# Optimization experiments

Hardware: AMD Instinct MI355X
Metric: run time of the kernel (lower is better)

The kernel has to match this reference:

```python
import jax, jax.numpy as jnp
import numpy as np

PAD = 0
C_CONST = 0.1712209


def setup_inputs() -> dict:
    key = jax.random.key(0)
    ks = jax.random.split(key, 6)
    tlen, bsz, slen, hsize, vocab = 64, 32, 64, 1024, 32000
    hidden = jax.random.normal(ks[0], (tlen, bsz, hsize), dtype=jnp.float32)
    context = jax.random.normal(ks[1], (slen, bsz, hsize), dtype=jnp.float32)
    src = jax.random.randint(ks[2], (bsz, slen), 0, vocab, dtype=jnp.int64)
    stdv = 1.0 / np.sqrt(hsize)
    W_gen = jax.random.uniform(ks[3], (vocab, hsize), dtype=jnp.float32, minval=-stdv, maxval=stdv)
    b_gen = jnp.zeros((vocab,), dtype=jnp.float32)
    # Xavier-like init for the copy gate
    w_copy = jax.random.normal(ks[4], (hsize,), dtype=jnp.float32) * np.sqrt(2.0 / (hsize + 1))
    b_copy = jnp.zeros((1,), dtype=jnp.float32)
    return {"hidden": hidden, "context": context, "src": src,
            "W_gen": W_gen, "b_gen": b_gen, "w_copy": w_copy, "b_copy": b_copy}


def reference(hidden, context, src, W_gen, b_gen, w_copy, b_copy):
    tlen, bsz, hsize = hidden.shape
    # p(z=1): probability of copying, [tlen, bsz, 1]
    copy_prob = jax.nn.sigmoid(jnp.einsum('tbh,h->tb', hidden, w_copy) + b_copy[0])[..., None]
    # generator distribution over tgt vocab
    logits = jnp.einsum('tbh,vh->tbv', hidden, W_gen) + b_gen
    prob = jax.nn.softmax(logits.astype(jnp.float32), axis=-1)
    p_g = prob * (1.0 - copy_prob)  # [tlen, bsz, vocab]
    # copy attention over source positions: bmm(query[b,t,h], keys[b,s,h]^T)
    attn_score = jnp.einsum('tbh,sbh->bts', hidden, context)  # [bsz, tlen, slen]
    src_mask = (src == PAD)[:, None, :]  # [bsz, 1, slen]
    attn_score = jnp.where(src_mask, -jnp.inf, attn_score.astype(jnp.float32))
    attns = jax.nn.softmax(attn_score, axis=-1)  # [bsz, tlen, slen]
    p_c = jnp.transpose(attns, (1, 0, 2)) * copy_prob  # [tlen, bsz, slen]
    # scatter_add copy probs into vocab distribution along dim 2
    slen = src.shape[1]
    idx_src = jnp.broadcast_to(src[None, :, :], (tlen, bsz, slen))
    t_idx = jnp.arange(tlen)[:, None, None]
    b_idx = jnp.arange(bsz)[None, :, None]
    p_g = p_g.at[t_idx, b_idx, idx_src].add(p_c)
    return jnp.log(p_g) + C_CONST
```

## Files before the change

### kernel.cpp

```cpp
#include <hip/hip_runtime.h>
#include <hip/hip_bf16.h>
#include <stdint.h>

#define TLEN 64
#define BSZ 32
#define SLEN 64
#define HS 1024
#define VOC 32000
#define NROW (TLEN*BSZ)
#define C_CONST_F 0.1712209f

#define BM 256
#define BN 256
#define BKT 32
#define NKT (HS/BKT)
#define SLOT_BYTES 32768
#define B_REGION 16384

typedef __attribute__((ext_vector_type(8))) short short8;
typedef __attribute__((ext_vector_type(4))) float f32x4;

static __device__ __forceinline__ ushort f2bf(float f) {
    uint32_t u = __builtin_bit_cast(uint32_t, f);
    uint32_t r = (u + 0x7fffu + ((u >> 16) & 1u)) >> 16;
    return (ushort)r;
}
static __device__ __forceinline__ float bf2f(ushort u) {
    uint32_t v = ((uint32_t)u) << 16;
    return __builtin_bit_cast(float, v);
}
static __device__ __forceinline__ void async16(const void* g, void* lds) {
    __builtin_amdgcn_global_load_lds(
        (const __attribute__((address_space(1))) void*)g,
        (__attribute__((address_space(3))) void*)lds, 16, 0, 0);
}
static __device__ __forceinline__ int swz12(int e) { return e ^ (((e >> 4) & 15) << 1); }

__global__ __launch_bounds__(256) void gate_kernel(const float* __restrict__ hidden,
                                                   const float* __restrict__ w_copy,
                                                   const float* __restrict__ b_copy,
                                                   float* __restrict__ cp) {
    int wid = threadIdx.x >> 6, lane = threadIdx.x & 63;
    int row = blockIdx.x * 4 + wid;
    const float* h = hidden + (size_t)row * HS;
    float acc = 0.f;
    for (int i = 0; i < 4; ++i) {
        int off = (i * 64 + lane) * 4;
        float4 a = *(const float4*)(h + off);
        float4 w = *(const float4*)(w_copy + off);
        acc += a.x * w.x + a.y * w.y + a.z * w.z + a.w * w.w;
    }
    for (int m = 32; m >= 1; m >>= 1) acc += __shfl_xor(acc, m, 64);
    if (lane == 0) cp[row] = 1.f / (1.f + expf(-(acc + b_copy[0])));
}

__global__ __launch_bounds__(256) void attn_kernel(const float* __restrict__ hidden,
                                                   const float* __restrict__ context,
                                                   const int* __restrict__ src,
                                                   const float* __restrict__ cp,
                                                   float* __restrict__ p_c) {
    int row = blockIdx.x;
    int b = row & (BSZ - 1);
    int tid = threadIdx.x, wid = tid >> 6, lane = tid & 63;
    __shared__ float hrow[HS];
    __shared__ float sc[SLEN];
    *(float4*)(hrow + tid * 4) = *(const float4*)(hidden + (size_t)row * HS + tid * 4);
    __syncthreads();
    for (int j = 0; j < 16; ++j) {
        int s = wid * 16 + j;
        const float* c = context + ((size_t)s * BSZ + b) * HS;
        float acc = 0.f;
        for (int i = 0; i < 4; ++i) {
            int off = (i * 64 + lane) * 4;
            float4 cv = *(const float4*)(c + off);
            float4 hv = *(const float4*)(hrow + off);
            acc += cv.x * hv.x + cv.y * hv.y + cv.z * hv.z + cv.w * hv.w;
        }
        for (int m = 32; m >= 1; m >>= 1) acc += __shfl_xor(acc, m, 64);
        if (lane == 0) sc[s] = acc;
    }
    __syncthreads();
    if (tid < SLEN) {
        float v = sc[tid];
        if (src[b * SLEN + tid] == 0) v = -INFINITY;
        float m = v;
        for (int k = 32; k >= 1; k >>= 1) m = fmaxf(m, __shfl_xor(m, k, 64));
        float e = expf(v - m);
        float ssum = e;
        for (int k = 32; k >= 1; k >>= 1) ssum += __shfl_xor(ssum, k, 64);
        p_c[row * SLEN + tid] = (e / ssum) * cp[row];
    }
}

__global__ __launch_bounds__(256) void cvt_kernel(const float* __restrict__ in,
                                                  ushort* __restrict__ out, int n4) {
    int i = blockIdx.x * blockDim.x + threadIdx.x;
    if (i >= n4) return;
    float4 v = ((const float4*)in)[i];
    ushort4 o;
    o.x = f2bf(v.x); o.y = f2bf(v.y); o.z = f2bf(v.z); o.w = f2bf(v.w);
    ((ushort4*)out)[i] = o;
}

template <bool BF16L>
__global__ __launch_bounds__(512, 2) void gemm_kernel(const ushort* __restrict__ A,
                                                      const ushort* __restrict__ B,
                                                      const float* __restrict__ b_gen,
                                                      void* __restrict__ logits,
                                                      float* __restrict__ partials ) {
    __shared__ ushort sAB[4 * SLOT_BYTES / 2];

    int orig = blockIdx.x;
    int wg = (orig & 7) * 125 + (orig >> 3);
    int mIdx = wg & 7;
    int nIdx = wg >> 3;
    int m0 = mIdx * BM, n0 = nIdx * BN;
    int tid = threadIdx.x, wid = tid >> 6, lane = tid & 63;
    int wm = (wid >> 2) * 128, wn = (wid & 3) * 64;
    int lr = lane & 15, lg = lane >> 4;

    const ushort* gA[2]; const ushort* gB[2];
    uint32_t ldsOffA[2], ldsOffB[2];
    #pragma unroll
    for (int j = 0; j < 2; ++j) {
        int s = j * 512 + tid;
        int row = s >> 2;
        int kc = (s & 3) ^ ((row >> 1) & 3);
        gA[j] = A + (size_t)(m0 + row) * HS + kc * 8;
        gB[j] = B + (size_t)(n0 + row) * HS + kc * 8;
        ldsOffA[j] = (uint32_t)((j * 512 + wid * 64) * 16);
        ldsOffB[j] = (uint32_t)(B_REGION + (j * 512 + wid * 64) * 16);
    }

    uint32_t kcs   = (uint32_t)((lg ^ ((lr >> 1) & 3)) * 16);
    uint32_t offAb = (uint32_t)(wm + lr) * 64 + kcs;
    uint32_t offBb = B_REGION + (uint32_t)(wn + lr) * 64 + kcs;

    f32x4 acc[8][4];
    #pragma unroll
    for (int m = 0; m < 8; ++m)
        #pragma unroll
        for (int n = 0; n < 4; ++n) acc[m][n] = f32x4{0.f, 0.f, 0.f, 0.f};

    for (int kt = 0; kt < 3; ++kt) {
        char* sd = (char*)sAB + kt * SLOT_BYTES;
        int k0 = kt * BKT;
        #pragma unroll
        for (int j = 0; j < 2; ++j) {
            async16(gA[j] + k0, sd + ldsOffA[j]);
            async16(gB[j] + k0, sd + ldsOffB[j]);
        }
    }

#define PHASE_BODY(KT, DOSTAGE)                                                        \
    {                                                                                  \
        const char* sl = (const char*)sAB + ((KT) & 3) * SLOT_BYTES;                   \
        short8 af[8], bv[4];                                                           \
        _Pragma("unroll")                                                              \
        for (int mb = 0; mb < 8; ++mb)                                                 \
            af[mb] = *(const short8*)(sl + offAb + mb * 1024);                         \
        _Pragma("unroll")                                                              \
        for (int nb = 0; nb < 4; ++nb)                                                 \
            bv[nb] = *(const short8*)(sl + offBb + nb * 1024);                         \
        if (DOSTAGE) {                                                                 \
            char* sd = (char*)sAB + (((KT) + 3) & 3) * SLOT_BYTES;                     \
            int k0s = ((KT) + 3) * BKT;                                                \
            _Pragma("unroll")                                                          \
            for (int j = 0; j < 2; ++j) {                                              \
                async16(gA[j] + k0s, sd + ldsOffA[j]);                                 \
                async16(gB[j] + k0s, sd + ldsOffB[j]);                                 \
            }                                                                          \
        }                                                                              \
        __builtin_amdgcn_s_setprio(1);                                                 \
        _Pragma("unroll")                                                              \
        for (int mb = 0; mb < 8; ++mb)                                                 \
            _Pragma("unroll")                                                          \
            for (int nb = 0; nb < 4; ++nb)                                             \
                acc[mb][nb] = __builtin_amdgcn_mfma_f32_16x16x32_bf16(af[mb], bv[nb],  \
                                                                     acc[mb][nb], 0, 0, 0); \
        __builtin_amdgcn_s_setprio(0);                                                 \
    }

    for (int kt = 0; kt < NKT - 3; ++kt) {
        asm volatile("s_waitcnt vmcnt(8)\n\ts_barrier" ::: "memory");
        PHASE_BODY(kt, true);
    }
    asm volatile("s_waitcnt vmcnt(8)\n\ts_barrier" ::: "memory");
    PHASE_BODY(NKT - 3, false);
    asm volatile("s_waitcnt vmcnt(4)\n\ts_barrier" ::: "memory");
    PHASE_BODY(NKT - 2, false);
    asm volatile("s_waitcnt vmcnt(0)\n\ts_barrier" ::: "memory");
    PHASE_BODY(NKT - 1, false);
#undef PHASE_BODY

    asm volatile("s_barrier" ::: "memory");

    float bg[4];
    #pragma unroll
    for (int nb = 0; nb < 4; ++nb) bg[nb] = b_gen[n0 + wn + nb * 16 + lr];
    int chunk = nIdx * 4 + (wid & 3);
    ushort* stile = sAB + wid * 8192;

    #pragma unroll
    for (int mb = 0; mb < 8; ++mb) {
        #pragma unroll
        for (int r = 0; r < 4; ++r) {
            int rl = mb * 16 + lg * 4 + r;
            int row = m0 + wm + rl;
            float v[4];
            float mx = -INFINITY;
            #pragma unroll
            for (int nb = 0; nb < 4; ++nb) {
                v[nb] = acc[mb][nb][r] + bg[nb];
                mx = fmaxf(mx, v[nb]);
            }
            if (BF16L) {
                #pragma unroll
                for (int nb = 0; nb < 4; ++nb) {
                    int cl = nb * 16 + lr;
                    int slot_w = (cl >> 3) ^ (rl & 7);
                    stile[rl * 64 + slot_w * 8 + (cl & 7)] = f2bf(v[nb]);
                }
            } else {
                float* outp = (float*)logits;
                #pragma unroll
                for (int nb = 0; nb < 4; ++nb)
                    outp[(size_t)row * VOC + n0 + wn + nb * 16 + lr] = v[nb];
            }
            for (int k = 8; k >= 1; k >>= 1) mx = fmaxf(mx, __shfl_xor(mx, k, 16));
            float se = 0.f;
            #pragma unroll
            for (int nb = 0; nb < 4; ++nb) se += __expf(v[nb] - mx);
            for (int k = 8; k >= 1; k >>= 1) se += __shfl_xor(se, k, 16);
            if (lr == 0) {
                float2 pv; pv.x = mx; pv.y = se;
                *(float2*)(partials + ((size_t)row * 500 + chunk) * 2) = pv;
            }
        }
    }
    if (BF16L) {
        ushort* Lbf = (ushort*)logits;
        #pragma unroll
        for (int rep = 0; rep < 16; ++rep) {
            int idx = rep * 64 + lane;
            int rl = idx >> 3, c8 = idx & 7;
            int slot_r = c8 ^ (rl & 7);
            short8 val = *(const short8*)(stile + rl * 64 + slot_r * 8);
            ushort* dst = Lbf + (size_t)(m0 + wm + rl) * VOC + n0 + wn + c8 * 8;
            *(short8*)dst = val;
        }
    }
}

__global__ __launch_bounds__(256) void reduce_kernel(const float* __restrict__ partials,
                                                     float* __restrict__ Ms,
                                                     float* __restrict__ Ss) {
    int wid = threadIdx.x >> 6, lane = threadIdx.x & 63;
    int row = blockIdx.x * 4 + wid;
    float m = -INFINITY, s = 0.f;
    for (int c = lane; c < 500; c += 64) {
        float2 p = *(const float2*)(partials + ((size_t)row * 500 + c) * 2);
        float nm = fmaxf(m, p.x);
        s = s * __expf(m - nm) + p.y * __expf(p.x - nm);
        m = nm;
    }
    for (int k = 32; k >= 1; k >>= 1) {
        float om = __shfl_xor(m, k, 64), os = __shfl_xor(s, k, 64);
        float nm = fmaxf(m, om);
        s = s * __expf(m - nm) + os * __expf(om - nm);
        m = nm;
    }
    if (lane == 0) { Ms[row] = m; Ss[row] = s; }
}

template <bool BF16L>
__global__ __launch_bounds__(256) void finalize_kernel(const int* __restrict__ src,
                                                       const float* __restrict__ p_c,
                                                       const float* __restrict__ cp,
                                                       const float* __restrict__ Ms,
                                                       const float* __restrict__ Ss,
                                                       const void* __restrict__ logits,
                                                       float* __restrict__ out) {
    int row = blockIdx.y;
    int c0 = blockIdx.x * 4096;
    int b = row & (BSZ - 1);
    __shared__ float addv[4096];
    int tid = threadIdx.x;
    for (int i = tid; i < 4096; i += 256) addv[i] = 0.f;
    __syncthreads();
    if (tid < SLEN) {
        int v = src[b * SLEN + tid];
        if (v >= c0 && v < c0 + 4096)
            atomicAdd(&addv[swz12(v - c0)], p_c[row * SLEN + tid]);
    }
    __syncthreads();
    int col = c0 + tid * 16;
    if (col >= VOC) return;
    float M = Ms[row];
    float g = (1.f - cp[row]) / Ss[row];
    float L[16];
    if (BF16L) {
        const ushort* lb = (const ushort*)logits + (size_t)row * VOC + col;
        short8 a = *(const short8*)lb;
        short8 c = *(const short8*)(lb + 8);
        for (int i = 0; i < 8; ++i) { L[i] = bf2f((ushort)a[i]); L[8 + i] = bf2f((ushort)c[i]); }
    } else {
        const float* lf = (const float*)logits + (size_t)row * VOC + col;
        for (int i = 0; i < 4; ++i) {
            float4 v = *(const float4*)(lf + i * 4);
            L[i * 4 + 0] = v.x; L[i * 4 + 1] = v.y; L[i * 4 + 2] = v.z; L[i * 4 + 3] = v.w;
        }
    }
    float res[16];
    for (int i = 0; i < 16; ++i) {
        float p = __expf(L[i] - M) * g + addv[swz12(tid * 16 + i)];
        res[i] = __logf(p) + C_CONST_F;
    }
    float* op = out + (size_t)row * VOC + col;
    for (int i = 0; i < 4; ++i) {
        float4 v;
        v.x = res[i * 4 + 0]; v.y = res[i * 4 + 1]; v.z = res[i * 4 + 2]; v.w = res[i * 4 + 3];
        *(float4*)(op + i * 4) = v;
    }
}

extern "C" void kernel_launch(void* const* d_in, const int* in_sizes, int n_in,
                              void* d_out, int out_size, void* d_ws, size_t ws_size,
                              hipStream_t stream) {
    const float* hidden  = (const float*)d_in[0];
    const float* context = (const float*)d_in[1];
    const int*   src     = (const int*)d_in[2];
    const float* W_gen   = (const float*)d_in[3];
    const float* b_gen   = (const float*)d_in[4];
    const float* w_copy  = (const float*)d_in[5];
    const float* b_copy  = (const float*)d_in[6];
    float* out = (float*)d_out;
    char* ws = (char*)d_ws;

    float*  cp       = (float*)(ws);
    float*  p_c      = (float*)(ws + 8192);
    float*  Ms       = (float*)(ws + 532480);
    float*  Ss       = (float*)(ws + 540672);
    float*  partials = (float*)(ws + 548864);
    ushort* Abf      = (ushort*)(ws + 8740864);
    ushort* Wbf      = (ushort*)(ws + 12935168);
    ushort* Lbf      = (ushort*)(ws + 78471168);
    const size_t NEED_BF16 = 209543168;

    gate_kernel<<<NROW / 4, 256, 0, stream>>>(hidden, w_copy, b_copy, cp);
    attn_kernel<<<NROW, 256, 0, stream>>>(hidden, context, src, cp, p_c);
    cvt_kernel<<<(NROW * HS / 4) / 256, 256, 0, stream>>>(hidden, Abf, NROW * HS / 4);
    cvt_kernel<<<(VOC * HS / 4) / 256, 256, 0, stream>>>(W_gen, Wbf, VOC * HS / 4);

    int ggrid = (NROW / BM) * (VOC / BN);
    dim3 fgrid(8, NROW);
    if (ws_size >= NEED_BF16) {
        gemm_kernel<true><<<ggrid, 512, 0, stream>>>(Abf, Wbf, b_gen, Lbf, partials);
        reduce_kernel<<<NROW / 4, 256, 0, stream>>>(partials, Ms, Ss);
        finalize_kernel<true><<<fgrid, 256, 0, stream>>>(src, p_c, cp, Ms, Ss, Lbf, out);
    } else {
        gemm_kernel<false><<<ggrid, 512, 0, stream>>>(Abf, Wbf, b_gen, out, partials);
        reduce_kernel<<<NROW / 4, 256, 0, stream>>>(partials, Ms, Ss);
        finalize_kernel<false><<<fgrid, 256, 0, stream>>>(src, p_c, cp, Ms, Ss, out, out);
    }
}
```

Measured before the change: 342.1 us.

## Split each K-tile into two half-phases with ping-pong barrier scheduling

Each K-tile's MFMA work is split into two halves of 4 M-blocks. Each half loads its own A fragments, and the async global-to-LDS loads for the next stage are issued in two parts. Explicit s_barrier, lgkmcnt waits and sched_barriers separate LDS reads from MFMA clusters, in the style of a ping-pong/interleaved schedule. This halves the A-fragment register footprint and is meant to overlap memory traffic with compute across waves, at the cost of more barriers per K-tile.

```diff
diff --git a/kernel.cpp b/kernel.cpp
--- a/kernel.cpp
+++ b/kernel.cpp
@@ -151,49 +151,68 @@
             async16(gB[j] + k0, sd + ldsOffB[j]);
         }
     }
-
-#define PHASE_BODY(KT, DOSTAGE)                                                        \
+    asm volatile("s_waitcnt vmcnt(8)" ::: "memory");
+    asm volatile("s_barrier" ::: "memory");
+
+#define KTILE(KT, DOSTAGE, VMASM)                                                      \
     {                                                                                  \
         const char* sl = (const char*)sAB + ((KT) & 3) * SLOT_BYTES;                   \
-        short8 af[8], bv[4];                                                           \
-        _Pragma("unroll")                                                              \
-        for (int mb = 0; mb < 8; ++mb)                                                 \
-            af[mb] = *(const short8*)(sl + offAb + mb * 1024);                         \
+        short8 av[4], bv[4];                                                           \
         _Pragma("unroll")                                                              \
         for (int nb = 0; nb < 4; ++nb)                                                 \
             bv[nb] = *(const short8*)(sl + offBb + nb * 1024);                         \
+        _Pragma("unroll")                                                              \
+        for (int mb = 0; mb < 4; ++mb)                                                 \
+            av[mb] = *(const short8*)(sl + offAb + mb * 1024);                         \
         if (DOSTAGE) {                                                                 \
             char* sd = (char*)sAB + (((KT) + 3) & 3) * SLOT_BYTES;                     \
             int k0s = ((KT) + 3) * BKT;                                                \
-            _Pragma("unroll")                                                          \
-            for (int j = 0; j < 2; ++j) {                                              \
-                async16(gA[j] + k0s, sd + ldsOffA[j]);                                 \
-                async16(gB[j] + k0s, sd + ldsOffB[j]);                                 \
-            }                                                                          \
+            async16(gA[0] + k0s, sd + ldsOffA[0]);                                     \
+            async16(gB[0] + k0s, sd + ldsOffB[0]);                                     \
         }                                                                              \
+        asm volatile("s_barrier" ::: "memory");                                        \
+        asm volatile("s_waitcnt lgkmcnt(0)" ::: "memory");                             \
+        __builtin_amdgcn_sched_barrier(0);                                             \
         __builtin_amdgcn_s_setprio(1);                                                 \
         _Pragma("unroll")                                                              \
-        for (int mb = 0; mb < 8; ++mb)                                                 \
+        for (int mb = 0; mb < 4; ++mb)                                                 \
             _Pragma("unroll")                                                          \
             for (int nb = 0; nb < 4; ++nb)                                             \
-                acc[mb][nb] = __builtin_amdgcn_mfma_f32_16x16x32_bf16(af[mb], bv[nb],  \
+                acc[mb][nb] = __builtin_amdgcn_mfma_f32_16x16x32_bf16(av[mb], bv[nb],  \
                                                                      acc[mb][nb], 0, 0, 0); \
         __builtin_amdgcn_s_setprio(0);                                                 \
+        asm volatile("s_barrier" ::: "memory");                                        \
+        _Pragma("unroll")                                                              \
+        for (int mb = 0; mb < 4; ++mb)                                                 \
+            av[mb] = *(const short8*)(sl + offAb + 4096 + mb * 1024);                  \
+        if (DOSTAGE) {                                                                 \
+            char* sd = (char*)sAB + (((KT) + 3) & 3) * SLOT_BYTES;                     \
+            int k0s = ((KT) + 3) * BKT;                                                \
+            async16(gA[1] + k0s, sd + ldsOffA[1]);                                     \
+            async16(gB[1] + k0s, sd + ldsOffB[1]);                                     \
+        }                                                                              \
+        VMASM;                                                                         \
+        asm volatile("s_barrier" ::: "memory");                                        \
+        asm volatile("s_waitcnt lgkmcnt(0)" ::: "memory");                             \
+        __builtin_amdgcn_sched_barrier(0);                                             \
+        __builtin_amdgcn_s_setprio(1);                                                 \
+        _Pragma("unroll")                                                              \
+        for (int mb = 0; mb < 4; ++mb)                                                 \
+            _Pragma("unroll")                                                          \
+            for (int nb = 0; nb < 4; ++nb)                                             \
+                acc[mb + 4][nb] = __builtin_amdgcn_mfma_f32_16x16x32_bf16(av[mb], bv[nb], \
+                                                                     acc[mb + 4][nb], 0, 0, 0); \
+        __builtin_amdgcn_s_setprio(0);                                                 \
+        asm volatile("s_barrier" ::: "memory");                                        \
     }
 
     for (int kt = 0; kt < NKT - 3; ++kt) {
-        asm volatile("s_waitcnt vmcnt(8)\n\ts_barrier" ::: "memory");
-        PHASE_BODY(kt, true);
-    }
-    asm volatile("s_waitcnt vmcnt(8)\n\ts_barrier" ::: "memory");
-    PHASE_BODY(NKT - 3, false);
-    asm volatile("s_waitcnt vmcnt(4)\n\ts_barrier" ::: "memory");
-    PHASE_BODY(NKT - 2, false);
-    asm volatile("s_waitcnt vmcnt(0)\n\ts_barrier" ::: "memory");
-    PHASE_BODY(NKT - 1, false);
-#undef PHASE_BODY
-
-    asm volatile("s_barrier" ::: "memory");
+        KTILE(kt, true, asm volatile("s_waitcnt vmcnt(8)" ::: "memory"));
+    }
+    KTILE(NKT - 3, false, asm volatile("s_waitcnt vmcnt(4)" ::: "memory"));
+    KTILE(NKT - 2, false, asm volatile("s_waitcnt vmcnt(0)" ::: "memory"));
+    KTILE(NKT - 1, false, );
+#undef KTILE
 
     float bg[4];
     #pragma unroll
```

After: 346.3 us. No clear change (+1.2%).

## Load A fragments directly from global into registers, stage only B in LDS

Applied to the files above, without the earlier changes.

The GEMM no longer stages the A (hidden) tile through LDS. Each lane now loads its A fragments straight from global memory into registers, one k-step ahead. Only B is staged into a 4-slot async LDS ring, and the waitcnt and barrier schedule is reworked to match. The aim is to halve LDS traffic and the staging work. In exchange, A fragments are loaded redundantly across waves (each A row is read by the 4 waves sharing it) and global load latency is exposed with only one step of register prefetch.

```diff
diff --git a/kernel.cpp b/kernel.cpp
--- a/kernel.cpp
+++ b/kernel.cpp
@@ -14,8 +14,7 @@
 #define BN 256
 #define BKT 32
 #define NKT (HS/BKT)
-#define SLOT_BYTES 32768
-#define B_REGION 16384
+#define SLOT_B 16384
 
 typedef __attribute__((ext_vector_type(8))) short short8;
 typedef __attribute__((ext_vector_type(4))) float f32x4;
@@ -108,7 +107,7 @@
                                                       const float* __restrict__ b_gen,
                                                       void* __restrict__ logits,
                                                       float* __restrict__ partials ) {
-    __shared__ ushort sAB[4 * SLOT_BYTES / 2];
+    __shared__ ushort sAB[65536];
 
     int orig = blockIdx.x;
     int wg = (orig & 7) * 125 + (orig >> 3);
@@ -119,22 +118,24 @@
     int wm = (wid >> 2) * 128, wn = (wid & 3) * 64;
     int lr = lane & 15, lg = lane >> 4;
 
-    const ushort* gA[2]; const ushort* gB[2];
-    uint32_t ldsOffA[2], ldsOffB[2];
+    const ushort* gB[2];
+    uint32_t ldsOffB[2];
     #pragma unroll
     for (int j = 0; j < 2; ++j) {
         int s = j * 512 + tid;
         int row = s >> 2;
         int kc = (s & 3) ^ ((row >> 1) & 3);
-        gA[j] = A + (size_t)(m0 + row) * HS + kc * 8;
         gB[j] = B + (size_t)(n0 + row) * HS + kc * 8;
-        ldsOffA[j] = (uint32_t)((j * 512 + wid * 64) * 16);
-        ldsOffB[j] = (uint32_t)(B_REGION + (j * 512 + wid * 64) * 16);
-    }
-
-    uint32_t kcs   = (uint32_t)((lg ^ ((lr >> 1) & 3)) * 16);
-    uint32_t offAb = (uint32_t)(wm + lr) * 64 + kcs;
-    uint32_t offBb = B_REGION + (uint32_t)(wn + lr) * 64 + kcs;
+        ldsOffB[j] = (uint32_t)((j * 512 + wid * 64) * 16);
+    }
+
+    uint32_t kcs  = (uint32_t)((lg ^ ((lr >> 1) & 3)) * 16);
+    uint32_t offBb = (uint32_t)(wn + lr) * 64 + kcs;
+
+    const ushort* aRow[8];
+    #pragma unroll
+    for (int mb = 0; mb < 8; ++mb)
+        aRow[mb] = A + (size_t)(m0 + wm + mb * 16 + lr) * HS + lg * 8;
 
     f32x4 acc[8][4];
     #pragma unroll
@@ -142,58 +143,57 @@
         #pragma unroll
         for (int n = 0; n < 4; ++n) acc[m][n] = f32x4{0.f, 0.f, 0.f, 0.f};
 
-    for (int kt = 0; kt < 3; ++kt) {
-        char* sd = (char*)sAB + kt * SLOT_BYTES;
-        int k0 = kt * BKT;
-        #pragma unroll
-        for (int j = 0; j < 2; ++j) {
-            async16(gA[j] + k0, sd + ldsOffA[j]);
-            async16(gB[j] + k0, sd + ldsOffB[j]);
-        }
-    }
-
-#define PHASE_BODY(KT, DOSTAGE)                                                        \
-    {                                                                                  \
-        const char* sl = (const char*)sAB + ((KT) & 3) * SLOT_BYTES;                   \
-        short8 af[8], bv[4];                                                           \
-        _Pragma("unroll")                                                              \
-        for (int mb = 0; mb < 8; ++mb)                                                 \
-            af[mb] = *(const short8*)(sl + offAb + mb * 1024);                         \
-        _Pragma("unroll")                                                              \
-        for (int nb = 0; nb < 4; ++nb)                                                 \
-            bv[nb] = *(const short8*)(sl + offBb + nb * 1024);                         \
-        if (DOSTAGE) {                                                                 \
-            char* sd = (char*)sAB + (((KT) + 3) & 3) * SLOT_BYTES;                     \
-            int k0s = ((KT) + 3) * BKT;                                                \
-            _Pragma("unroll")                                                          \
-            for (int j = 0; j < 2; ++j) {                                              \
-                async16(gA[j] + k0s, sd + ldsOffA[j]);                                 \
-                async16(gB[j] + k0s, sd + ldsOffB[j]);                                 \
-            }                                                                          \
-        }                                                                              \
-        __builtin_amdgcn_s_setprio(1);                                                 \
-        _Pragma("unroll")                                                              \
-        for (int mb = 0; mb < 8; ++mb)                                                 \
-            _Pragma("unroll")                                                          \
-            for (int nb = 0; nb < 4; ++nb)                                             \
-                acc[mb][nb] = __builtin_amdgcn_mfma_f32_16x16x32_bf16(af[mb], bv[nb],  \
-                                                                     acc[mb][nb], 0, 0, 0); \
-        __builtin_amdgcn_s_setprio(0);                                                 \
-    }
-
-    for (int kt = 0; kt < NKT - 3; ++kt) {
-        asm volatile("s_waitcnt vmcnt(8)\n\ts_barrier" ::: "memory");
-        PHASE_BODY(kt, true);
-    }
-    asm volatile("s_waitcnt vmcnt(8)\n\ts_barrier" ::: "memory");
-    PHASE_BODY(NKT - 3, false);
-    asm volatile("s_waitcnt vmcnt(4)\n\ts_barrier" ::: "memory");
-    PHASE_BODY(NKT - 2, false);
-    asm volatile("s_waitcnt vmcnt(0)\n\ts_barrier" ::: "memory");
-    PHASE_BODY(NKT - 1, false);
-#undef PHASE_BODY
-
+#define STAGE_B(KT)                                                        \
+    {                                                                      \
+        char* sd = (char*)sAB + ((KT) & 3) * SLOT_B;                       \
+        int k0s = (KT) * BKT;                                              \
+        async16(gB[0] + k0s, sd + ldsOffB[0]);                             \
+        async16(gB[1] + k0s, sd + ldsOffB[1]);                             \
+    }
+
+    short8 av[8];
+    STAGE_B(0);
+    __builtin_amdgcn_sched_barrier(0);
+    #pragma unroll
+    for (int mb = 0; mb < 8; ++mb) av[mb] = *(const short8*)(aRow[mb]);
+    __builtin_amdgcn_sched_barrier(0);
+    STAGE_B(1);
+    STAGE_B(2);
+    asm volatile("s_waitcnt vmcnt(12)" ::: "memory");
     asm volatile("s_barrier" ::: "memory");
+
+    for (int kt = 0; kt < NKT; ++kt) {
+        const char* sl = (const char*)sAB + (kt & 3) * SLOT_B;
+        short8 bv[4];
+        #pragma unroll
+        for (int nb = 0; nb < 4; ++nb)
+            bv[nb] = *(const short8*)(sl + offBb + nb * 1024);
+        if (kt < NKT - 3) {
+            STAGE_B(kt + 3);
+            asm volatile("s_waitcnt vmcnt(2)" ::: "memory");
+        } else {
+            asm volatile("s_waitcnt vmcnt(0)" ::: "memory");
+        }
+        asm volatile("s_waitcnt lgkmcnt(0)" ::: "memory");
+        __builtin_amdgcn_sched_barrier(0);
+        __builtin_amdgcn_s_setprio(1);
+        #pragma unroll
+        for (int mb = 0; mb < 8; ++mb)
+            #pragma unroll
+            for (int nb = 0; nb < 4; ++nb)
+                acc[mb][nb] = __builtin_amdgcn_mfma_f32_16x16x32_bf16(av[mb], bv[nb],
+                                                                     acc[mb][nb], 0, 0, 0);
+        __builtin_amdgcn_s_setprio(0);
+        if (kt < NKT - 1) {
+            const ushort* ak = (const ushort*)((const char*)0 + (kt + 1) * (BKT * 2));
+            #pragma unroll
+            for (int mb = 0; mb < 8; ++mb)
+                av[mb] = *(const short8*)(aRow[mb] + (kt + 1) * BKT);
+            (void)ak;
+        }
+        asm volatile("s_barrier" ::: "memory");
+    }
+#undef STAGE_B
 
     float bg[4];
     #pragma unroll
```

After: 509.5 us. 1.49x slower.
